# Optimization experiments

Hardware: AMD Instinct MI355X
Metric: run time of the kernel (lower is better)

Reference implementation:

```python
import jax, jax.numpy as jnp
import numpy as np

N, D = 8192, 256
TEMPERATURE = 1.0
K_NEIGHBORS = 5  # min(5, N-1)
EPS = 1e-08


def setup_inputs() -> dict:
    key = jax.random.key(0)
    k1, k2 = jax.random.split(key)
    node_embeddings = jax.random.normal(k1, (N, D), dtype=jnp.float32)
    adj_matrix = jax.random.uniform(k2, (N, N), dtype=jnp.float32)
    return {"node_embeddings": node_embeddings, "adj_matrix": adj_matrix}


def _components(node_embeddings, adj_matrix):
    n = node_embeddings.shape[0]

    # --- total energy ---
    kinetic = jnp.sum(node_embeddings ** 2, axis=-1)  # [N]
    neighbor_emb = adj_matrix @ node_embeddings       # [N, D]
    potential = -jnp.sum(node_embeddings * neighbor_emb, axis=-1)
    degrees = jnp.sum(adj_matrix, axis=-1)
    total_energy = kinetic + potential / (degrees + EPS)

    # --- local entropy (cosine sims masked by adjacency, softmax rowwise) ---
    norms = jnp.linalg.norm(node_embeddings, axis=-1, keepdims=True)
    normalized = node_embeddings / jnp.maximum(norms, 1e-12)  # F.normalize eps
    similarities = normalized @ normalized.T                  # [N, N]
    masked = similarities * adj_matrix
    row_sums = jnp.sum(adj_matrix, axis=1)
    probs = jax.nn.softmax(masked / TEMPERATURE, axis=1)
    ent = -jnp.sum(probs * jnp.log(probs + EPS), axis=1)
    local_entropy = jnp.where(row_sums > 0, ent, 0.0)

    # --- equilibrium deviation (global + KNN-local) ---
    global_mean = jnp.mean(node_embeddings, axis=0, keepdims=True)
    global_dev = jnp.linalg.norm(node_embeddings - global_mean, axis=-1)
    sq = jnp.sum(node_embeddings ** 2, axis=-1)
    d2 = sq[:, None] + sq[None, :] - 2.0 * (node_embeddings @ node_embeddings.T)
    dist = jnp.sqrt(jnp.maximum(d2, 0.0))  # torch.cdist equivalent
    _, topk_idx = jax.lax.top_k(-dist, K_NEIGHBORS + 1)  # smallest k+1
    neighbor_idx = topk_idx[:, 1:]                        # drop self, [N, K]
    local_means = jnp.mean(node_embeddings[neighbor_idx], axis=1)  # [N, D]
    local_dev = jnp.linalg.norm(node_embeddings - local_means, axis=-1)
    equilibrium_deviation = 0.6 * global_dev + 0.4 * local_dev

    # --- structural centrality ---
    degree_centrality = degrees / (n - 1 + EPS)
    emb_norms = jnp.linalg.norm(node_embeddings, axis=-1)
    emb_centrality = emb_norms / (jnp.max(emb_norms) + EPS)
    structural_centrality = 0.5 * degree_centrality + 0.5 * emb_centrality

    return jnp.stack([total_energy, local_entropy, equilibrium_deviation, structural_centrality])  # [4, N]


def reference(node_embeddings, adj_matrix):
    return _components(node_embeddings, adj_matrix)
```

## Files before the change

kernel.cpp:

```cpp
#include <hip/hip_runtime.h>
#include <math.h>

#define N 8192
#define D 256
#define EPSF 1e-8f
#define NJS 8
#define ROWS 32
#define JSPAN 1024
#define NCH 32

#define WS_SQ    0
#define WS_RINV  (N)
#define WS_GMEAN (2*N)
#define WS_MAXN  (2*N+256)
#define WS_COLP  (2*N+512)
#define WS_P0    (2*N+512+65536)
#define WS_EBF   (WS_P0+80*N)

typedef __attribute__((ext_vector_type(8))) short bf16x8;
typedef __attribute__((ext_vector_type(4))) float f32x4;

__device__ __forceinline__ unsigned short f2bf(float f) {
    unsigned u = __float_as_uint(f);
    u += 0x7fffu + ((u >> 16) & 1u);
    return (unsigned short)(u >> 16);
}

#if __has_builtin(__builtin_amdgcn_exp2f)
#define EXP2(x) __builtin_amdgcn_exp2f(x)
#else
#define EXP2(x) exp2f(x)
#endif

#if __has_builtin(__builtin_amdgcn_fmed3f)
#define MED3(a,b,c) __builtin_amdgcn_fmed3f((a),(b),(c))
#else
#define MED3(a,b,c) fmaxf(fminf((a),(b)), fminf(fmaxf((a),(b)),(c)))
#endif

#define PINS6(T, x) do {                                                        \
    float _x = (x);                                                             \
    float _n0 = fminf((T)[0], _x);                                              \
    float _n1 = MED3((T)[0], (T)[1], _x);                                       \
    float _n2 = MED3((T)[1], (T)[2], _x);                                       \
    float _n3 = MED3((T)[2], (T)[3], _x);                                       \
    float _n4 = MED3((T)[3], (T)[4], _x);                                       \
    float _n5 = MED3((T)[4], (T)[5], _x);                                       \
    (T)[0]=_n0; (T)[1]=_n1; (T)[2]=_n2; (T)[3]=_n3; (T)[4]=_n4; (T)[5]=_n5;     \
  } while (0)

__global__ void k_prep(const float* __restrict__ emb, float* __restrict__ ws,
                       unsigned short* __restrict__ ebf) {
    if (blockIdx.x < 2048) {
        int row = blockIdx.x * 4 + (threadIdx.x >> 6);
        int lane = threadIdx.x & 63;
        float4 v = *(const float4*)(emb + (size_t)row * D + lane * 4);
        ushort4 b;
        b.x = f2bf(v.x); b.y = f2bf(v.y); b.z = f2bf(v.z); b.w = f2bf(v.w);
        *(ushort4*)(ebf + (size_t)row * D + lane * 4) = b;
        float s = v.x * v.x + v.y * v.y + v.z * v.z + v.w * v.w;
#pragma unroll
        for (int mk = 32; mk >= 1; mk >>= 1) s += __shfl_xor(s, mk);
        if (lane == 0) {
            ws[WS_SQ + row] = s;
            ws[WS_RINV + row] = 1.0f / fmaxf(sqrtf(s), 1e-12f);
        }
    } else {
        int d = threadIdx.x;
        int b = blockIdx.x - 2048;
        float s = 0.f;
        for (int r = b * 32; r < b * 32 + 32; ++r) s += emb[(size_t)r * D + d];
        ws[WS_COLP + b * 256 + d] = s;
    }
}

__global__ void k_colred(float* __restrict__ ws) {
    __shared__ float red[256];
    int d = threadIdx.x;
    float s = 0.f;
    for (int b = 0; b < 256; ++b) s += ws[WS_COLP + b * 256 + d];
    ws[WS_GMEAN + d] = s * (1.0f / N);
    float mx = 0.f;
    for (int i = d; i < N; i += 256) mx = fmaxf(mx, ws[WS_SQ + i]);
    red[d] = mx;
    __syncthreads();
#pragma unroll
    for (int st2 = 128; st2 >= 1; st2 >>= 1) {
        if (d < st2) red[d] = fmaxf(red[d], red[d + st2]);
        __syncthreads();
    }
    if (d == 0) ws[WS_MAXN] = sqrtf(red[0]);
}

#define STAGE(PTR, SOFF, K0) do {                                               \
    _Pragma("unroll")                                                           \
    for (int q = 0; q < 4; ++q) {                                               \
      __builtin_amdgcn_global_load_lds(                                         \
        (const __attribute__((address_space(1))) void*)(ebf + gbase + (SOFF) + (K0) + q * (8 * D)), \
        (__attribute__((address_space(3))) void*)&(PTR)[(q << 3) * 64],         \
        16, 0, 0);                                                              \
    } } while (0)

#define VMW(NLIT) do {                                                          \
    asm volatile("s_waitcnt vmcnt(" #NLIT ")" ::: "memory");                    \
    __builtin_amdgcn_sched_barrier(0);                                          \
  } while (0)

#define SBAR() __builtin_amdgcn_sched_barrier(0)

#define COMP(PTR, H) do {                                                       \
    _Pragma("unroll")                                                           \
    for (int ksl = 0; ksl < 2; ++ksl) {                                         \
      const int pg = ((ksl << 2) + g) ^ (lid & 7);                              \
      bf16x8 afr[2];                                                            \
      _Pragma("unroll")                                                         \
      for (int mf = 0; mf < 2; ++mf)                                            \
        afr[mf] = *(const bf16x8*)&(PTR)[((mf << 4) + lid) * 64 + (pg << 3)];   \
      _Pragma("unroll")                                                         \
      for (int nf = 0; nf < 2; ++nf)                                            \
        _Pragma("unroll")                                                       \
        for (int mf = 0; mf < 2; ++mf)                                          \
          acc[nf][mf] = __builtin_amdgcn_mfma_f32_16x16x32_bf16(                \
              afr[mf], bfr[nf][(H) * 2 + ksl],                                  \
              ((H) == 0 && ksl == 0) ? z4 : acc[nf][mf], 0, 0, 0);              \
    } } while (0)

__global__ __launch_bounds__(64, 2) void k_main(
    const float* __restrict__ adj,
    const unsigned short* __restrict__ ebf,
    const float* __restrict__ ws,
    float* __restrict__ pout)
{
    __shared__ unsigned short tile0[32 * 64];
    __shared__ unsigned short tile1[32 * 64];
    __shared__ unsigned short tile2[32 * 64];
    __shared__ unsigned short tile3[32 * 64];

    const int l = threadIdx.x;
    const int lid = l & 15;
    const int g = l >> 4;
    const int srow = l >> 3;
    const int sc = (l & 7) ^ srow;
    const int panel = blockIdx.x >> 3;
    const int js = blockIdx.x & 7;
    const int row0 = panel * ROWS;
    const int j0 = js * JSPAN;

    const float* sq = ws + WS_SQ;
    const float* rinv = ws + WS_RINV;
    const size_t gbase = (size_t)(j0 + srow) * D + (sc << 3);
    const f32x4 z4 = (f32x4){0.f, 0.f, 0.f, 0.f};

    bf16x8 bfr[2][8];
    float rvr2[2];
    int r_[2];
#pragma unroll
    for (int nf = 0; nf < 2; ++nf) {
        int r = row0 + nf * 16 + lid;
        r_[nf] = r;
        rvr2[nf] = rinv[r] * 1.44269504f;
#pragma unroll
        for (int ks = 0; ks < 8; ++ks)
            bfr[nf][ks] = *(const bf16x8*)(ebf + (size_t)r * D + ks * 32 + g * 8);
    }

    float deg[2] = {0.f, 0.f}, pot[2] = {0.f, 0.f};
    float sl[2] = {0.f, 0.f}, st[2] = {0.f, 0.f};
    float tv[2][6];
#pragma unroll
    for (int nf = 0; nf < 2; ++nf)
#pragma unroll
        for (int s2 = 0; s2 < 6; ++s2) tv[nf][s2] = 1e30f;

    f32x4 acc[2][2];
#pragma unroll
    for (int nf = 0; nf < 2; ++nf)
#pragma unroll
        for (int mf = 0; mf < 2; ++mf) acc[nf][mf] = z4;
    f32x4 advA[2][2], sqv[2], rvv[2];

    STAGE(tile0, 0, 0);
    STAGE(tile1, 0, 64);
    STAGE(tile2, 0, 128);
    STAGE(tile3, 0, 192);

#pragma unroll 1
    for (int cc = 0; cc < NCH; ++cc) {
        const int jj = j0 + cc * 32;
        const size_t snext = (size_t)(cc + 1) * (32 * D);

#pragma unroll
        for (int nf = 0; nf < 2; ++nf)
#pragma unroll
            for (int mf = 0; mf < 2; ++mf)
                advA[nf][mf] = __builtin_nontemporal_load(
                    (const f32x4*)(adj + (size_t)r_[nf] * N + jj + mf * 16 + g * 4));
        VMW(16);
        COMP(tile0, 0);
        SBAR();
        STAGE(tile0, snext, 0);

#pragma unroll
        for (int mf = 0; mf < 2; ++mf) {
            sqv[mf] = *(const f32x4*)(sq + jj + mf * 16 + g * 4);
            rvv[mf] = *(const f32x4*)(rinv + jj + mf * 16 + g * 4);
        }
        VMW(20);
        COMP(tile1, 1);
        SBAR();
        STAGE(tile1, snext, 64);

        VMW(16);
        COMP(tile2, 2);
        SBAR();
        STAGE(tile2, snext, 128);

        VMW(8);
        COMP(tile3, 3);
        SBAR();
        STAGE(tile3, snext, 192);
#pragma unroll
        for (int nf = 0; nf < 2; ++nf) {
#pragma unroll
            for (int mf = 0; mf < 2; ++mf) {
#pragma unroll
                for (int e = 0; e < 4; ++e) {
                    const float gv = acc[nf][mf][e];
                    const float a = advA[nf][mf][e];
                    const int j = jj + mf * 16 + g * 4 + e;
                    deg[nf] += a;
                    pot[nf] = fmaf(a, gv, pot[nf]);
                    const float s2v = (gv * rvr2[nf]) * (rvv[mf][e] * a);
                    const float ex = EXP2(s2v);
                    sl[nf] += ex;
                    st[nf] = fmaf(ex, s2v, st[nf]);
                    const float dp = fmaf(-2.f, gv, sqv[mf][e]);
                    const float key = __uint_as_float(
                        (__float_as_uint(dp) & 0xFFFFE000u) | (unsigned)j);
                    PINS6(tv[nf], key);
                }
            }
        }
    }

#pragma unroll
    for (int nf = 0; nf < 2; ++nf) {
#pragma unroll
        for (int mk = 16; mk <= 32; mk <<= 1) {
            deg[nf] += __shfl_xor(deg[nf], mk);
            pot[nf] += __shfl_xor(pot[nf], mk);
            sl[nf] += __shfl_xor(sl[nf], mk);
            st[nf] += __shfl_xor(st[nf], mk);
            float ok[6];
#pragma unroll
            for (int s2 = 0; s2 < 6; ++s2) ok[s2] = __shfl_xor(tv[nf][s2], mk);
#pragma unroll
            for (int s2 = 0; s2 < 6; ++s2) PINS6(tv[nf], ok[s2]);
        }
        if (g == 0) {
            const int slot = js * N + row0 + nf * 16 + lid;
            pout[slot] = deg[nf];
            pout[8 * N + slot] = pot[nf];
            pout[16 * N + slot] = sl[nf];
            pout[24 * N + slot] = st[nf];
#pragma unroll
            for (int s2 = 0; s2 < 6; ++s2)
                pout[32 * N + (size_t)slot * 6 + s2] = tv[nf][s2];
        }
    }
}

__global__ void k_final(const float* __restrict__ emb, const float* __restrict__ ws,
                        float* __restrict__ out) {
    int row = blockIdx.x * 4 + (threadIdx.x >> 6);
    int lane = threadIdx.x & 63;
    const float* p0 = ws + WS_P0;

    float dg = 0.f, pt = 0.f, ll = 0.f, tt = 0.f;
#pragma unroll
    for (int js = 0; js < NJS; ++js) {
        int slot = js * N + row;
        dg += p0[slot]; pt += p0[8 * N + slot];
        ll += p0[16 * N + slot]; tt += p0[24 * N + slot];
    }

    float keys[6];
#pragma unroll
    for (int s = 0; s < 6; ++s) keys[s] = p0[32 * N + (size_t)row * 6 + s];
#pragma unroll
    for (int js = 1; js < NJS; ++js)
#pragma unroll
        for (int s = 0; s < 6; ++s)
            PINS6(keys, p0[32 * N + (size_t)(js * N + row) * 6 + s]);
    int nb[5];
#pragma unroll
    for (int t = 0; t < 5; ++t) nb[t] = (int)(__float_as_uint(keys[t + 1]) & 0x1FFFu);

    float4 e = *(const float4*)(emb + (size_t)row * D + lane * 4);
    float4 gm = *(const float4*)(ws + WS_GMEAN + lane * 4);
    float gx = e.x - gm.x, gy = e.y - gm.y, gz = e.z - gm.z, gw = e.w - gm.w;
    float gd = gx * gx + gy * gy + gz * gz + gw * gw;
    float ax = 0.f, ay = 0.f, az = 0.f, aw = 0.f;
#pragma unroll
    for (int t = 0; t < 5; ++t) {
        float4 nv = *(const float4*)(emb + (size_t)nb[t] * D + lane * 4);
        ax += nv.x; ay += nv.y; az += nv.z; aw += nv.w;
    }
    ax *= 0.2f; ay *= 0.2f; az *= 0.2f; aw *= 0.2f;
    float lx = e.x - ax, ly = e.y - ay, lz = e.z - az, lw = e.w - aw;
    float ld = lx * lx + ly * ly + lz * lz + lw * lw;
#pragma unroll
    for (int mk = 32; mk >= 1; mk >>= 1) {
        gd += __shfl_xor(gd, mk);
        ld += __shfl_xor(ld, mk);
    }
    if (lane == 0) {
        float sqv = ws[WS_SQ + row];
        float mn = ws[WS_MAXN];
        float ent = logf(ll) - (tt * 0.6931471805599453f) / ll;
        out[row] = sqv - pt / (dg + EPSF);
        out[N + row] = (dg > 0.f) ? ent : 0.f;
        out[2 * N + row] = 0.6f * sqrtf(gd) + 0.4f * sqrtf(ld);
        out[3 * N + row] = 0.5f * (dg / (8191.0f + EPSF)) + 0.5f * (sqrtf(sqv) / (mn + EPSF));
    }
}

extern "C" void kernel_launch(void* const* d_in, const int* in_sizes, int n_in,
                              void* d_out, int out_size, void* d_ws, size_t ws_size,
                              hipStream_t stream) {
    const float* emb = (const float*)d_in[0];
    const float* adj = (const float*)d_in[1];
    float* out = (float*)d_out;
    float* ws = (float*)d_ws;
    unsigned short* ebf = (unsigned short*)(ws + WS_EBF);

    k_prep<<<2304, 256, 0, stream>>>(emb, ws, ebf);
    k_colred<<<1, 256, 0, stream>>>(ws);
    k_main<<<2048, 64, 0, stream>>>(adj, ebf, ws, ws + WS_P0);
    k_final<<<N / 4, 256, 0, stream>>>(emb, ws, out);
}
```

Before: 165.1 us.

## Double-buffer adjacency and column vectors to prefetch one chunk ahead

Adjacency tiles and the sq/rinv column vectors are now loaded one 32-column chunk ahead into ping-pong register sets. The loop is unrolled by two so the buffers alternate without copies. The goal is to hide the global-load latency of adj behind the MFMA work of the previous chunk instead of waiting on it within the same chunk. This costs extra VGPRs, which could pressure occupancy under launch_bounds(64,2), and the vmcnt waits were retuned to match.

```diff
diff --git a/kernel.cpp b/kernel.cpp
--- a/kernel.cpp
+++ b/kernel.cpp
@@ -125,6 +125,63 @@
               ((H) == 0 && ksl == 0) ? z4 : acc[nf][mf], 0, 0, 0);              \
     } } while (0)
 
+#define PREF(AX, SQX, RVX, JPF) do {                                            \
+    _Pragma("unroll")                                                           \
+    for (int nf = 0; nf < 2; ++nf)                                              \
+      _Pragma("unroll")                                                         \
+      for (int mf = 0; mf < 2; ++mf)                                            \
+        AX[nf][mf] = __builtin_nontemporal_load(                                \
+            (const f32x4*)(adj + (size_t)r_[nf] * N + (JPF) + mf * 16 + g * 4));\
+    _Pragma("unroll")                                                           \
+    for (int mf = 0; mf < 2; ++mf) {                                            \
+      SQX[mf] = *(const f32x4*)(sq + (JPF) + mf * 16 + g * 4);                  \
+      RVX[mf] = *(const f32x4*)(rinv + (JPF) + mf * 16 + g * 4);                \
+    } } while (0)
+
+#define CHUNK(CC, AC, SQC, RVC, AN, SQN, RVN) do {                              \
+    const int jj = j0 + (CC) * 32;                                              \
+    const int jpf = ((CC) < NCH - 1) ? jj + 32 : jj;   \
+    const size_t snext = (size_t)((CC) + 1) * (32 * D);                         \
+    PREF(AN, SQN, RVN, jpf);                                                    \
+    VMW(20);                                                                    \
+    COMP(tile0, 0);                                                             \
+    SBAR();                                                                     \
+    STAGE(tile0, snext, 0);                                                     \
+    VMW(20);                                                                    \
+    COMP(tile1, 1);                                                             \
+    SBAR();                                                                     \
+    STAGE(tile1, snext, 64);                                                    \
+    VMW(20);                                                                    \
+    COMP(tile2, 2);                                                             \
+    SBAR();                                                                     \
+    STAGE(tile2, snext, 128);                                                   \
+    VMW(20);                                                                    \
+    COMP(tile3, 3);                                                             \
+    SBAR();                                                                     \
+    STAGE(tile3, snext, 192);                                                   \
+    _Pragma("unroll")                                                           \
+    for (int nf = 0; nf < 2; ++nf) {                                            \
+      _Pragma("unroll")                                                         \
+      for (int mf = 0; mf < 2; ++mf) {                                          \
+        _Pragma("unroll")                                                       \
+        for (int e = 0; e < 4; ++e) {                                           \
+          const float gv = acc[nf][mf][e];                                      \
+          const float a = AC[nf][mf][e];                                        \
+          const int j = jj + mf * 16 + g * 4 + e;                               \
+          deg[nf] += a;                                                         \
+          pot[nf] = fmaf(a, gv, pot[nf]);                                       \
+          const float s2v = (gv * rvr2[nf]) * (RVC[mf][e] * a);                 \
+          const float ex = EXP2(s2v);                                           \
+          sl[nf] += ex;                                                         \
+          st[nf] = fmaf(ex, s2v, st[nf]);                                       \
+          const float dp = fmaf(-2.f, gv, SQC[mf][e]);                          \
+          const float key = __uint_as_float(                                    \
+              (__float_as_uint(dp) & 0xFFFFE000u) | (unsigned)j);               \
+          PINS6(tv[nf], key);                                                   \
+        }                                                                       \
+      }                                                                         \
+    } } while (0)
+
 __global__ __launch_bounds__(64, 2) void k_main(
     const float* __restrict__ adj,
     const unsigned short* __restrict__ ebf,
@@ -177,70 +234,20 @@
     for (int nf = 0; nf < 2; ++nf)
 #pragma unroll
         for (int mf = 0; mf < 2; ++mf) acc[nf][mf] = z4;
-    f32x4 advA[2][2], sqv[2], rvv[2];
-
+
+    f32x4 aA[2][2], sqA[2], rvA[2];
+    f32x4 aB[2][2], sqB[2], rvB[2];
+
+    PREF(aA, sqA, rvA, j0);
     STAGE(tile0, 0, 0);
     STAGE(tile1, 0, 64);
     STAGE(tile2, 0, 128);
     STAGE(tile3, 0, 192);
 
 #pragma unroll 1
-    for (int cc = 0; cc < NCH; ++cc) {
-        const int jj = j0 + cc * 32;
-        const size_t snext = (size_t)(cc + 1) * (32 * D);
-
-#pragma unroll
-        for (int nf = 0; nf < 2; ++nf)
-#pragma unroll
-            for (int mf = 0; mf < 2; ++mf)
-                advA[nf][mf] = __builtin_nontemporal_load(
-                    (const f32x4*)(adj + (size_t)r_[nf] * N + jj + mf * 16 + g * 4));
-        VMW(16);
-        COMP(tile0, 0);
-        SBAR();
-        STAGE(tile0, snext, 0);
-
-#pragma unroll
-        for (int mf = 0; mf < 2; ++mf) {
-            sqv[mf] = *(const f32x4*)(sq + jj + mf * 16 + g * 4);
-            rvv[mf] = *(const f32x4*)(rinv + jj + mf * 16 + g * 4);
-        }
-        VMW(20);
-        COMP(tile1, 1);
-        SBAR();
-        STAGE(tile1, snext, 64);
-
-        VMW(16);
-        COMP(tile2, 2);
-        SBAR();
-        STAGE(tile2, snext, 128);
-
-        VMW(8);
-        COMP(tile3, 3);
-        SBAR();
-        STAGE(tile3, snext, 192);
-#pragma unroll
-        for (int nf = 0; nf < 2; ++nf) {
-#pragma unroll
-            for (int mf = 0; mf < 2; ++mf) {
-#pragma unroll
-                for (int e = 0; e < 4; ++e) {
-                    const float gv = acc[nf][mf][e];
-                    const float a = advA[nf][mf][e];
-                    const int j = jj + mf * 16 + g * 4 + e;
-                    deg[nf] += a;
-                    pot[nf] = fmaf(a, gv, pot[nf]);
-                    const float s2v = (gv * rvr2[nf]) * (rvv[mf][e] * a);
-                    const float ex = EXP2(s2v);
-                    sl[nf] += ex;
-                    st[nf] = fmaf(ex, s2v, st[nf]);
-                    const float dp = fmaf(-2.f, gv, sqv[mf][e]);
-                    const float key = __uint_as_float(
-                        (__float_as_uint(dp) & 0xFFFFE000u) | (unsigned)j);
-                    PINS6(tv[nf], key);
-                }
-            }
-        }
+    for (int cc = 0; cc < NCH; cc += 2) {
+        CHUNK(cc, aA, sqA, rvA, aB, sqB, rvB);
+        CHUNK(cc + 1, aB, sqB, rvB, aA, sqA, rvA);
     }
 
 #pragma unroll
```

Result: no change. 162.7 us (-1.5%).
